# Kernel optimization log

Hardware: AMD Instinct MI355X
Metric: run time of the kernel (lower is better)

The kernel has to match this reference:

```python
import jax, jax.numpy as jnp
import numpy as np

N_QUBITS = 16
DIM = 1 << N_QUBITS
NUM_CLASSES = 23
BATCH = 64

# PauliZ sign table: wire 0 is the most-significant bit of the flattened index.
_idx = np.arange(DIM)
SIGNS = np.stack([1 - 2 * ((_idx >> (N_QUBITS - 1 - w)) & 1) for w in range(N_QUBITS)], axis=1).astype(np.float32)  # (DIM, 16)


def _rx_mat(theta):
    c = jnp.cos(theta / 2).astype(jnp.complex64)
    s = (-1j * jnp.sin(theta / 2)).astype(jnp.complex64)
    return jnp.stack([jnp.stack([c, s]), jnp.stack([s, c])])  # (2,2)


def _rot_mat(phi, theta, omega):
    ct = jnp.cos(theta / 2)
    st = jnp.sin(theta / 2)
    a = jnp.exp(-0.5j * (phi + omega)) * ct
    b = -jnp.exp(0.5j * (phi - omega)) * st
    c = jnp.exp(-0.5j * (phi - omega)) * st
    d = jnp.exp(0.5j * (phi + omega)) * ct
    return jnp.stack([jnp.stack([a, b]), jnp.stack([c, d])]).astype(jnp.complex64)


def _apply_1q(state, U, w):
    # state: (B, 2,...,2); shared 2x2 gate on wire w (axis w+1)
    st = jnp.tensordot(state, U, axes=[[w + 1], [1]])  # contracted axis moves to last
    return jnp.moveaxis(st, -1, w + 1)


def _apply_rx_batched(state, theta_b, w):
    # per-sample RX angles theta_b: (B,)
    half = theta_b / 2
    c = jnp.cos(half).astype(jnp.complex64)
    s = (-1j * jnp.sin(half)).astype(jnp.complex64)
    U = jnp.stack([jnp.stack([c, s], -1), jnp.stack([s, c], -1)], -2)  # (B,2,2)
    st = jnp.moveaxis(state, w + 1, -1)
    st = jnp.einsum('bji,b...i->b...j', U, st)
    return jnp.moveaxis(st, -1, w + 1)


def _apply_crx(state, theta, ctrl, tgt):
    s0 = jax.lax.index_in_dim(state, 0, axis=ctrl + 1, keepdims=False)
    s1 = jax.lax.index_in_dim(state, 1, axis=ctrl + 1, keepdims=False)
    tax = tgt + 1 if tgt < ctrl else tgt  # target axis after control axis removal
    U = _rx_mat(theta)
    s1 = jnp.moveaxis(jnp.tensordot(s1, U, axes=[[tax], [1]]), -1, tax)
    return jnp.stack([s0, s1], axis=ctrl + 1)


def _circuit(x, w0, x0, w1, x1):
    B = x.shape[0]
    state = jnp.zeros((B,) + (2,) * N_QUBITS, jnp.complex64)
    state = state.at[(slice(None),) + (0,) * N_QUBITS].set(1.0)
    for w, xc in ((w0, x0), (w1, x1)):
        for q in range(N_QUBITS):
            state = _apply_rx_batched(state, x[:, q], q)
        for q in range(N_QUBITS):
            state = _apply_1q(state, _rot_mat(w[q, 0], w[q, 1], w[q, 2]), q)
        for q in range(N_QUBITS):
            state = _apply_crx(state, xc[q], q, (q + 1) % N_QUBITS)
    probs = (state.real ** 2 + state.imag ** 2).reshape(B, DIM)
    return probs @ jnp.asarray(SIGNS)  # (B, 16) PauliZ expvals


def setup_inputs() -> dict:
    key = jax.random.key(0)
    ks = jax.random.split(key, 7)
    return {
        'x': jax.random.normal(ks[0], (BATCH, N_QUBITS), jnp.float32),
        'w0': jax.random.normal(ks[1], (N_QUBITS, 3), jnp.float32),
        'x0': jax.random.normal(ks[2], (N_QUBITS,), jnp.float32),
        'w1': jax.random.normal(ks[3], (N_QUBITS, 3), jnp.float32),
        'x1': jax.random.normal(ks[4], (N_QUBITS,), jnp.float32),
        'fc_w': jax.random.normal(ks[5], (NUM_CLASSES, N_QUBITS), jnp.float32) * 0.25,
        'fc_b': jax.random.normal(ks[6], (NUM_CLASSES,), jnp.float32) * 0.05,
    }


def reference(x, w0, x0, w1, x1, fc_w, fc_b):
    feats = _circuit(x, w0, x0, w1, x1)           # (B, 16)
    logits = feats @ fc_w.T + fc_b                # (B, 23)
    return jax.nn.log_softmax(logits, axis=1)
```

## Files before the change

kernel.cpp:

```cpp
#include <hip/hip_runtime.h>
#include <hip/hip_bf16.h>


#define DIM 65536
#define BATCH 64
#define PSTR 548


template<int RB>
__device__ __forceinline__ void g1q_reg(float* sr, float* si, const float* U) {
  float u00r=U[0],u00i=U[1],u01r=U[2],u01i=U[3],u10r=U[4],u10i=U[5],u11r=U[6],u11i=U[7];
#pragma unroll
  for (int k = 0; k < 8; ++k) {
    int lo = k & ((1<<RB)-1);
    int j0 = ((k >> RB) << (RB+1)) | lo;
    int j1 = j0 | (1<<RB);
    float a0r=sr[j0], a0i=si[j0], a1r=sr[j1], a1i=si[j1];
    sr[j0] = u00r*a0r - u00i*a0i + u01r*a1r - u01i*a1i;
    si[j0] = u00r*a0i + u00i*a0r + u01r*a1i + u01i*a1r;
    sr[j1] = u10r*a0r - u10i*a0i + u11r*a1r - u11i*a1i;
    si[j1] = u10r*a0i + u10i*a0r + u11r*a1i + u11i*a1r;
  }
}

template<int RB, int CB>
__device__ __forceinline__ void gsel_reg_cc(float* sr, float* si, const float* M0, const float* M1) {
  float a0=M0[0],a1=M0[1],a2=M0[2],a3=M0[3],a4=M0[4],a5=M0[5],a6=M0[6],a7=M0[7];
  float b0=M1[0],b1=M1[1],b2=M1[2],b3=M1[3],b4=M1[4],b5=M1[5],b6=M1[6],b7=M1[7];
#pragma unroll
  for (int k = 0; k < 8; ++k) {
    int lo = k & ((1<<RB)-1);
    int j0 = ((k >> RB) << (RB+1)) | lo;
    int j1 = j0 | (1<<RB);
    const bool c = ((j0 >> CB) & 1) != 0;
    float u00r=c?b0:a0, u00i=c?b1:a1, u01r=c?b2:a2, u01i=c?b3:a3;
    float u10r=c?b4:a4, u10i=c?b5:a5, u11r=c?b6:a6, u11i=c?b7:a7;
    float p0r=sr[j0], p0i=si[j0], p1r=sr[j1], p1i=si[j1];
    sr[j0] = u00r*p0r - u00i*p0i + u01r*p1r - u01i*p1i;
    si[j0] = u00r*p0i + u00i*p0r + u01r*p1i + u01i*p1r;
    sr[j1] = u10r*p0r - u10i*p0i + u11r*p1r - u11i*p1i;
    si[j1] = u10r*p0i + u10i*p0r + u11r*p1i + u11i*p1r;
  }
}

template<int RB>
__device__ __forceinline__ void gsel_reg_pred(float* sr, float* si, const float* M0,
                                              const float* M1, bool ctrl) {
  float u[8];
#pragma unroll
  for (int e = 0; e < 8; ++e) u[e] = ctrl ? M1[e] : M0[e];
  g1q_reg<RB>(sr, si, u);
}

template<int LB, int CB>
__device__ __forceinline__ void gsel_lane_creg(float* sr, float* si, const float* M0,
                                               const float* M1, int lane) {
  int side = (lane >> LB) & 1;
  float d0r = side ? M0[6] : M0[0], d0i = side ? M0[7] : M0[1];
  float o0r = side ? M0[4] : M0[2], o0i = side ? M0[5] : M0[3];
  float d1r = side ? M1[6] : M1[0], d1i = side ? M1[7] : M1[1];
  float o1r = side ? M1[4] : M1[2], o1i = side ? M1[5] : M1[3];
#pragma unroll
  for (int j = 0; j < 16; ++j) {
    const bool c = ((j >> CB) & 1) != 0;
    float dr = c ? d1r : d0r, di = c ? d1i : d0i;
    float og = c ? o1r : o0r, oi = c ? o1i : o0i;
    float pr = __shfl_xor(sr[j], 1<<LB, 64);
    float pi = __shfl_xor(si[j], 1<<LB, 64);
    float mr = sr[j], mi = si[j];
    sr[j] = dr*mr - di*mi + og*pr - oi*pi;
    si[j] = dr*mi + di*mr + og*pi + oi*pr;
  }
}

template<int CB, int LB>
__device__ __forceinline__ void crx_reg_lane(float* sr, float* si, float c, float s) {
#pragma unroll
  for (int k = 0; k < 8; ++k) {
    int lo2 = k & ((1<<CB)-1);
    int j = ((((k >> CB) << (CB+1)) | lo2)) | (1<<CB);
    float pr = __shfl_xor(sr[j], 1<<LB, 64);
    float pi = __shfl_xor(si[j], 1<<LB, 64);
    float mr = sr[j], mi = si[j];
    sr[j] = c*mr + s*pi;
    si[j] = c*mi - s*pr;
  }
}

__device__ __forceinline__ int swz(int o) { return o ^ ((o>>4)&15) ^ ((o>>8)&15); }

__device__ __forceinline__ unsigned bfp(float r, float i) {
  unsigned ur = __float_as_uint(r), ui = __float_as_uint(i);
  ur = (ur + 0x7fffu + ((ur >> 16) & 1u)) >> 16;
  ui = (ui + 0x7fffu + ((ui >> 16) & 1u)) & 0xffff0000u;
  return (ur & 0xffffu) | ui;
}
__device__ __forceinline__ float bfr(unsigned u) { return __uint_as_float(u << 16); }
__device__ __forceinline__ float bfi(unsigned u) { return __uint_as_float(u & 0xffff0000u); }

#define MP(Pb, l, q, s) ((Pb) + (((l)*16+(q))*2+(s))*8)


__global__ __launch_bounds__(512) void pA(float4* __restrict__ cst4, float* __restrict__ P,
                                          const float* __restrict__ x, const float* __restrict__ w0,
                                          const float* __restrict__ x0, const float* __restrict__ w1,
                                          const float* __restrict__ x1, float* __restrict__ feats,
                                          int* __restrict__ ctr) {
  __shared__ float2 lds2[8192];
  int b = blockIdx.x;
  int t = threadIdx.x, lane = t & 63, wv = t >> 6;
  float* Pb = P + (size_t)b * PSTR;

  {
    float (*su)[8] = reinterpret_cast<float(*)[8]>(lds2);
    if (t < 16) feats[b*16 + t] = 0.f;
    if (t == 16) ctr[b] = 0;
    if (t < 32) {
      int l = t >> 4, q = t & 15;
      const float* W = (l ? w1 : w0) + q*3;
      float xa = 0.5f * x[b*16 + q];
      float cr = cosf(xa), sx = sinf(xa);
      float phi = W[0], th = W[1], om = W[2];
      float ct = cosf(0.5f*th), stt = sinf(0.5f*th);
      float po = 0.5f*(phi+om), pm = 0.5f*(phi-om);
      float ar =  cosf(po)*ct,  ai = -sinf(po)*ct;
      float br = -cosf(pm)*stt, bi = -sinf(pm)*stt;
      float cr2 = cosf(pm)*stt, ci2 = -sinf(pm)*stt;
      float dr =  cosf(po)*ct,  di =  sinf(po)*ct;
      float U[8];
      U[0] = ar*cr + bi*sx;   U[1] = ai*cr - br*sx;
      U[2] = ai*sx + br*cr;   U[3] = -ar*sx + bi*cr;
      U[4] = cr2*cr + di*sx;  U[5] = ci2*cr - dr*sx;
      U[6] = ci2*sx + dr*cr;  U[7] = -cr2*sx + di*cr;
      float* M0 = MP(Pb, l, q, 0);
      float* M1 = M0 + 8;
#pragma unroll
      for (int e = 0; e < 8; ++e) { M0[e] = U[e]; su[t][e] = U[e]; }
      if (q == 0) {
        float ang = l ? 0.5f*x0[15] : 0.f;
        float cg = cosf(ang), sg = sinf(ang);
        M1[0] =  cg*U[0] + sg*U[3];  M1[1] = cg*U[1] - sg*U[2];
        M1[2] =  sg*U[1] + cg*U[2];  M1[3] = -sg*U[0] + cg*U[3];
        M1[4] =  cg*U[4] + sg*U[7];  M1[5] = cg*U[5] - sg*U[6];
        M1[6] =  sg*U[5] + cg*U[6];  M1[7] = -sg*U[4] + cg*U[7];
      } else {
        float ang = 0.5f*(l ? x1[q-1] : x0[q-1]);
        float cg = cosf(ang), sg = sinf(ang);
        M1[0] = cg*U[0] + sg*U[5];  M1[1] = cg*U[1] - sg*U[4];
        M1[2] = cg*U[2] + sg*U[7];  M1[3] = cg*U[3] - sg*U[6];
        M1[4] = cg*U[4] + sg*U[1];  M1[5] = cg*U[5] - sg*U[0];
        M1[6] = cg*U[6] + sg*U[3];  M1[7] = cg*U[7] - sg*U[2];
      }
      if (t == 0) { Pb[546] = cosf(0.5f*x1[15]); Pb[547] = sinf(0.5f*x1[15]); }
    }
    __syncthreads();
    if (t == 0) {
      float T0r[8], T0i[8], T1r[8], T1i[8];
#pragma unroll
      for (int k = 0; k < 8; ++k) {
        int b2 = (k>>2)&1, b1 = (k>>1)&1, b0k = k&1;
        float xr = su[13][b2*4], xi = su[13][b2*4+1];
        float yr = su[14][b1*4], yi = su[14][b1*4+1];
        float zr = su[15][b0k*4], zi = su[15][b0k*4+1];
        float pr = xr*yr - xi*yi, pi = xr*yi + xi*yr;
        T0r[k] = pr*zr - pi*zi; T0i[k] = pr*zi + pi*zr;
      }
      float a12 = 0.5f*x0[12], c12 = cosf(a12), s12 = sinf(a12);
#pragma unroll
      for (int k = 0; k < 8; ++k) { T1r[k] = c12*T0r[k] + s12*T0i[k^4]; T1i[k] = c12*T0i[k] - s12*T0r[k^4]; }
      float a13 = 0.5f*x0[13], c13 = cosf(a13), s13 = sinf(a13);
      float n0r[8], n0i[8], n1r[8], n1i[8];
#pragma unroll
      for (int k = 0; k < 8; ++k) {
        if (k & 4) {
          n0r[k] = c13*T0r[k] + s13*T0i[k^2]; n0i[k] = c13*T0i[k] - s13*T0r[k^2];
          n1r[k] = c13*T1r[k] + s13*T1i[k^2]; n1i[k] = c13*T1i[k] - s13*T1r[k^2];
        } else { n0r[k]=T0r[k]; n0i[k]=T0i[k]; n1r[k]=T1r[k]; n1i[k]=T1i[k]; }
      }
      float a14 = 0.5f*x0[14], c14 = cosf(a14), s14 = sinf(a14);
      float* T0 = Pb + 512;
      float* T1 = Pb + 528;
#pragma unroll
      for (int k = 0; k < 8; ++k) {
        float r0, i0, r1, i1;
        if (k & 2) {
          r0 = c14*n0r[k] + s14*n0i[k^1]; i0 = c14*n0i[k] - s14*n0r[k^1];
          r1 = c14*n1r[k] + s14*n1i[k^1]; i1 = c14*n1i[k] - s14*n1r[k^1];
        } else { r0=n0r[k]; i0=n0i[k]; r1=n1r[k]; i1=n1i[k]; }
        T0[2*k] = r0; T0[2*k+1] = i0; T1[2*k] = r1; T1[2*k+1] = i1;
      }
    }
  }

  float sr[16], si[16];
#pragma unroll
  for (int r = 0; r < 16; ++r) { sr[r] = 0.f; si[r] = 0.f; }
  if (t == 0) sr[0] = 1.f;

  g1q_reg<3>(sr, si, MP(Pb,0,0,0));
  gsel_reg_cc<2,3>(sr, si, MP(Pb,0,1,0), MP(Pb,0,1,1));
  gsel_reg_cc<1,2>(sr, si, MP(Pb,0,2,0), MP(Pb,0,2,1));
  gsel_reg_cc<0,1>(sr, si, MP(Pb,0,3,0), MP(Pb,0,3,1));
  __syncthreads();
#pragma unroll
  for (int r = 0; r < 16; ++r) {
    int o = wv | (lane << 3) | (r << 9);
    lds2[swz(o)] = make_float2(sr[r], si[r]);
  }
  __syncthreads();
#pragma unroll
  for (int r = 0; r < 16; ++r) {
    int o = wv | (((lane>>4)&3) << 3) | (r << 5) | ((lane&15) << 9);
    float2 v = lds2[swz(o)]; sr[r] = v.x; si[r] = v.y;
  }
  gsel_reg_pred<3>(sr, si, MP(Pb,0,4,0), MP(Pb,0,4,1), (lane&1)!=0);
  gsel_reg_cc<2,3>(sr, si, MP(Pb,0,5,0), MP(Pb,0,5,1));
  gsel_reg_cc<1,2>(sr, si, MP(Pb,0,6,0), MP(Pb,0,6,1));
  gsel_reg_cc<0,1>(sr, si, MP(Pb,0,7,0), MP(Pb,0,7,1));
  __syncthreads();
#pragma unroll
  for (int r = 0; r < 16; ++r) {
    int o = wv | (((lane>>4)&3) << 3) | (r << 5) | ((lane&15) << 9);
    lds2[swz(o)] = make_float2(sr[r], si[r]);
  }
  __syncthreads();
#pragma unroll
  for (int r = 0; r < 16; ++r) {
    int o = (lane&1) | (r << 1) | (((lane>>1)&31) << 5) | (wv << 10);
    float2 v = lds2[swz(o)]; sr[r] = v.x; si[r] = v.y;
  }
  gsel_reg_pred<3>(sr, si, MP(Pb,0,8,0), MP(Pb,0,8,1), (lane&2)!=0);
  gsel_reg_cc<2,3>(sr, si, MP(Pb,0,9,0), MP(Pb,0,9,1));
  gsel_reg_cc<1,2>(sr, si, MP(Pb,0,10,0), MP(Pb,0,10,1));
  gsel_reg_cc<0,1>(sr, si, MP(Pb,0,11,0), MP(Pb,0,11,1));
  gsel_lane_creg<0,0>(sr, si, MP(Pb,0,12,0), MP(Pb,0,12,1), lane);
  __syncthreads();
#pragma unroll
  for (int r = 0; r < 16; ++r) {
    int o = (lane&1) | (r << 1) | (((lane>>1)&31) << 5) | (wv << 10);
    lds2[swz(o)] = make_float2(sr[r], si[r]);
  }
  __syncthreads();
#pragma unroll
  for (int r = 0; r < 16; ++r) {
    int o = ((wv>>2)&1) | (lane << 1) | ((wv&3) << 7) | (r << 9);
    float2 v = lds2[swz(o)]; sr[r] = v.x; si[r] = v.y;
  }
  {
    int base4 = (lane << 3) | ((wv&3) << 9) | (((wv>>2)&1) << 11);
    float4* dst = cst4 + (size_t)b*4096 + base4;
#pragma unroll
    for (int g = 0; g < 8; ++g)
      dst[g] = make_float4(sr[2*g], si[2*g], sr[2*g+1], si[2*g+1]);
  }
}


__global__ __launch_bounds__(512) void pB(unsigned* __restrict__ st, const float4* __restrict__ cst4,
                                          const float* __restrict__ P) {
  __shared__ float2 lds2[8192];
  int blk = blockIdx.x;
  int b = blk >> 3, m = blk & 7;
  int t = threadIdx.x, lane = t & 63, wv = t >> 6;
  const float* Pb = P + (size_t)b*PSTR;

  float sr[16], si[16];
  {
    const float4* src = cst4 + (size_t)b*4096 + ((lane << 3) | ((wv&3) << 9) | (((m>>2)&1) << 11));
    const float* Ts = ((m>>2)&1) ? (Pb + 528) : (Pb + 512);
    int k = ((wv>>2)&1) | ((m&1) << 1) | (((m>>1)&1) << 2);
    float tr = Ts[2*k], ti = Ts[2*k+1];
#pragma unroll
    for (int g = 0; g < 8; ++g) {
      float4 v = src[g];
      sr[2*g]   = tr*v.x - ti*v.y;  si[2*g]   = tr*v.y + ti*v.x;
      sr[2*g+1] = tr*v.z - ti*v.w;  si[2*g+1] = tr*v.w + ti*v.z;
    }
  }
  gsel_reg_pred<3>(sr, si, MP(Pb,1,0,0), MP(Pb,1,0,1), ((wv>>2)&1)!=0);
  gsel_reg_cc<2,3>(sr, si, MP(Pb,1,1,0), MP(Pb,1,1,1));
  gsel_reg_cc<1,2>(sr, si, MP(Pb,1,2,0), MP(Pb,1,2,1));
  gsel_reg_cc<0,1>(sr, si, MP(Pb,1,3,0), MP(Pb,1,3,1));
#pragma unroll
  for (int r = 0; r < 16; ++r) {
    int o = (lane&63) | ((wv&3) << 6) | (r << 8) | (((wv>>2)&1) << 12);
    lds2[swz(o)] = make_float2(sr[r], si[r]);
  }
  __syncthreads();
#pragma unroll
  for (int r = 0; r < 16; ++r) {
    int o = (lane&15) | (r << 4) | (((lane>>4)&3) << 8) | ((wv&3) << 10) | (((wv>>2)&1) << 12);
    float2 v = lds2[swz(o)]; sr[r] = v.x; si[r] = v.y;
  }
  gsel_reg_pred<3>(sr, si, MP(Pb,1,4,0), MP(Pb,1,4,1), (lane&16)!=0);
  gsel_reg_cc<2,3>(sr, si, MP(Pb,1,5,0), MP(Pb,1,5,1));
  gsel_reg_cc<1,2>(sr, si, MP(Pb,1,6,0), MP(Pb,1,6,1));
  gsel_reg_cc<0,1>(sr, si, MP(Pb,1,7,0), MP(Pb,1,7,1));
  __syncthreads();
#pragma unroll
  for (int r = 0; r < 16; ++r) {
    int o = (lane&15) | (r << 4) | (((lane>>4)&3) << 8) | ((wv&3) << 10) | (((wv>>2)&1) << 12);
    lds2[swz(o)] = make_float2(sr[r], si[r]);
  }
  __syncthreads();
#pragma unroll
  for (int r = 0; r < 16; ++r) {
    int o = r | ((lane&63) << 4) | ((wv&3) << 10) | (((wv>>2)&1) << 12);
    float2 v = lds2[swz(o)]; sr[r] = v.x; si[r] = v.y;
  }
  gsel_reg_pred<3>(sr, si, MP(Pb,1,8,0), MP(Pb,1,8,1), (lane&1)!=0);
  gsel_reg_cc<2,3>(sr, si, MP(Pb,1,9,0), MP(Pb,1,9,1));
  gsel_reg_cc<1,2>(sr, si, MP(Pb,1,10,0), MP(Pb,1,10,1));
  gsel_reg_cc<0,1>(sr, si, MP(Pb,1,11,0), MP(Pb,1,11,1));
  {
    int sbase = ((lane&63) << 4) | ((wv&3) << 10) | (((wv>>2)&1) << 12) | (m << 13);
    uint4* dst = (uint4*)(st + (size_t)b*DIM + sbase);
#pragma unroll
    for (int g = 0; g < 4; ++g)
      dst[g] = make_uint4(bfp(sr[4*g],si[4*g]), bfp(sr[4*g+1],si[4*g+1]),
                          bfp(sr[4*g+2],si[4*g+2]), bfp(sr[4*g+3],si[4*g+3]));
  }
}


__global__ __launch_bounds__(512) void p3(const unsigned* __restrict__ st, const float* __restrict__ P,
                                          float* __restrict__ feats, int* __restrict__ ctr,
                                          const float* __restrict__ fcw, const float* __restrict__ fcb,
                                          float* __restrict__ out) {
  int blk = blockIdx.x;
  int b = blk >> 3, n = blk & 7;
  int t = threadIdx.x, lane = t & 63, wv = t >> 6;
  const float* Pb = P + (size_t)b*PSTR;
  int base = (lane&31) | (wv << 5) | (n << 8) | ((lane>>5) << 11);
  const unsigned* S = st + (size_t)b*DIM + base;
  float sr[16], si[16];
#pragma unroll
  for (int r = 0; r < 16; ++r) { unsigned u = S[r << 12]; sr[r] = bfr(u); si[r] = bfi(u); }

  gsel_reg_pred<3>(sr, si, MP(Pb,1,12,0), MP(Pb,1,12,1), (lane&1)!=0);
  gsel_reg_cc<2,3>(sr, si, MP(Pb,1,13,0), MP(Pb,1,13,1));
  gsel_reg_cc<1,2>(sr, si, MP(Pb,1,14,0), MP(Pb,1,14,1));
  gsel_reg_cc<0,1>(sr, si, MP(Pb,1,15,0), MP(Pb,1,15,1));
  crx_reg_lane<0,5>(sr, si, Pb[546], Pb[547]);

  float tot=0.f, sA=0.f, sB=0.f, sC=0.f, sD=0.f;
#pragma unroll
  for (int r = 0; r < 16; ++r) {
    float p = sr[r]*sr[r] + si[r]*si[r];
    tot += p;
    sA += (r & 1) ? -p : p;
    sB += (r & 2) ? -p : p;
    sC += (r & 4) ? -p : p;
    sD += (r & 8) ? -p : p;
  }
  float f[16];
  f[15] = sA; f[14] = sB; f[13] = sC; f[12] = sD;
  f[11] = (lane&1)  ? -tot : tot;
  f[10] = (lane&2)  ? -tot : tot;
  f[9]  = (lane&4)  ? -tot : tot;
  f[8]  = (lane&8)  ? -tot : tot;
  f[7]  = (lane&16) ? -tot : tot;
  f[0]  = (lane&32) ? -tot : tot;
  f[6]  = (wv&1)    ? -tot : tot;
  f[5]  = (wv&2)    ? -tot : tot;
  f[4]  = (wv&4)    ? -tot : tot;
  f[3]  = (n&1)     ? -tot : tot;
  f[2]  = (n&2)     ? -tot : tot;
  f[1]  = (n&4)     ? -tot : tot;
#pragma unroll
  for (int w = 0; w < 16; ++w) {
#pragma unroll
    for (int off = 32; off; off >>= 1) f[w] += __shfl_xor(f[w], off, 64);
  }
  __shared__ float red[8][17];
  if (lane == 0) {
#pragma unroll
    for (int w = 0; w < 16; ++w) red[wv][w] = f[w];
  }
  __syncthreads();
  if (t < 16) {
    float acc = 0.f;
#pragma unroll
    for (int i = 0; i < 8; ++i) acc += red[i][t];
    atomicAdd(&feats[b*16 + t], acc);
  }

  __shared__ int flagS;
  __syncthreads();
  if (t == 0) { __threadfence(); flagS = atomicAdd(&ctr[b], 1); }
  __syncthreads();
  if (flagS == 7) {
    __shared__ float fs[16];
    __shared__ float lg[23];
    if (t < 16) fs[t] = __hip_atomic_load(&feats[b*16 + t], __ATOMIC_RELAXED, __HIP_MEMORY_SCOPE_AGENT);
    __syncthreads();
    if (t < 23) {
      float acc = fcb[t];
#pragma unroll
      for (int w = 0; w < 16; ++w) acc += fs[w] * fcw[t*16 + w];
      lg[t] = acc;
    }
    __syncthreads();
    if (t < 23) {
      float mx = -1e30f;
#pragma unroll
      for (int j = 0; j < 23; ++j) mx = fmaxf(mx, lg[j]);
      float Ssum = 0.f;
#pragma unroll
      for (int j = 0; j < 23; ++j) Ssum += expf(lg[j] - mx);
      out[b*23 + t] = lg[t] - mx - logf(Ssum);
    }
  }
}

extern "C" void kernel_launch(void* const* d_in, const int* in_sizes, int n_in,
                              void* d_out, int out_size, void* d_ws, size_t ws_size,
                              hipStream_t stream) {
  const float* x   = (const float*)d_in[0];
  const float* w0  = (const float*)d_in[1];
  const float* x0  = (const float*)d_in[2];
  const float* w1  = (const float*)d_in[3];
  const float* x1  = (const float*)d_in[4];
  const float* fcw = (const float*)d_in[5];
  const float* fcb = (const float*)d_in[6];
  float* out = (float*)d_out;

  char* ws = (char*)d_ws;
  unsigned* st  = (unsigned*)ws;
  float4* cst4  = (float4*)(ws + (size_t)BATCH * DIM * 4);
  float*  P     = (float*)((char*)cst4 + (size_t)BATCH * 8192 * 8);
  float*  feats = P + (size_t)BATCH * PSTR;
  int*    ctr   = (int*)(feats + BATCH*16);

  pA<<<BATCH, 512, 0, stream>>>(cst4, P, x, w0, x0, w1, x1, feats, ctr);
  pB<<<512, 512, 0, stream>>>(st, cst4, P);
  p3<<<512, 512, 0, stream>>>(st, P, feats, ctr, fcw, fcb, out);
  (void)in_sizes; (void)n_in; (void)out_size; (void)ws_size;
}
```

Before: 130.5 us.

## Fold layer-0 wire-12 gate into tail product factors, halve pA state

The layer-0 qubit-12 controlled gate (the lane-shuffle step plus its LDS transpose) is removed from pA. Because that gate acts on a factorised tail, it is folded into the precomputed product-state factor table T2, which pB applies when it loads the intermediate state. pA now handles a 4096-amplitude state with 256 threads, half the LDS, one fewer exchange round and half the global intermediate write and read. The cost is a larger per-sample parameter table and extra masking on the LDS index; correctness depends on the factorisation holding exactly.

```diff
diff --git a/kernel.cpp b/kernel.cpp
--- a/kernel.cpp
+++ b/kernel.cpp
@@ -4,7 +4,7 @@
 
 #define DIM 65536
 #define BATCH 64
-#define PSTR 548
+#define PSTR 580
 
 
 template<int RB>
@@ -52,27 +52,6 @@
   g1q_reg<RB>(sr, si, u);
 }
 
-template<int LB, int CB>
-__device__ __forceinline__ void gsel_lane_creg(float* sr, float* si, const float* M0,
-                                               const float* M1, int lane) {
-  int side = (lane >> LB) & 1;
-  float d0r = side ? M0[6] : M0[0], d0i = side ? M0[7] : M0[1];
-  float o0r = side ? M0[4] : M0[2], o0i = side ? M0[5] : M0[3];
-  float d1r = side ? M1[6] : M1[0], d1i = side ? M1[7] : M1[1];
-  float o1r = side ? M1[4] : M1[2], o1i = side ? M1[5] : M1[3];
-#pragma unroll
-  for (int j = 0; j < 16; ++j) {
-    const bool c = ((j >> CB) & 1) != 0;
-    float dr = c ? d1r : d0r, di = c ? d1i : d0i;
-    float og = c ? o1r : o0r, oi = c ? o1i : o0i;
-    float pr = __shfl_xor(sr[j], 1<<LB, 64);
-    float pi = __shfl_xor(si[j], 1<<LB, 64);
-    float mr = sr[j], mi = si[j];
-    sr[j] = dr*mr - di*mi + og*pr - oi*pi;
-    si[j] = dr*mi + di*mr + og*pi + oi*pr;
-  }
-}
-
 template<int CB, int LB>
 __device__ __forceinline__ void crx_reg_lane(float* sr, float* si, float c, float s) {
 #pragma unroll
@@ -101,12 +80,12 @@
 #define MP(Pb, l, q, s) ((Pb) + (((l)*16+(q))*2+(s))*8)
 
 
-__global__ __launch_bounds__(512) void pA(float4* __restrict__ cst4, float* __restrict__ P,
+__global__ __launch_bounds__(256) void pA(float2* __restrict__ pre2, float* __restrict__ P,
                                           const float* __restrict__ x, const float* __restrict__ w0,
                                           const float* __restrict__ x0, const float* __restrict__ w1,
                                           const float* __restrict__ x1, float* __restrict__ feats,
                                           int* __restrict__ ctr) {
-  __shared__ float2 lds2[8192];
+  __shared__ float2 lds2[4096];
   int b = blockIdx.x;
   int t = threadIdx.x, lane = t & 63, wv = t >> 6;
   float* Pb = P + (size_t)b * PSTR;
@@ -151,7 +130,7 @@
         M1[4] = cg*U[4] + sg*U[1];  M1[5] = cg*U[5] - sg*U[0];
         M1[6] = cg*U[6] + sg*U[3];  M1[7] = cg*U[7] - sg*U[2];
       }
-      if (t == 0) { Pb[546] = cosf(0.5f*x1[15]); Pb[547] = sinf(0.5f*x1[15]); }
+      if (t == 0) { Pb[576] = cosf(0.5f*x1[15]); Pb[577] = sinf(0.5f*x1[15]); }
     }
     __syncthreads();
     if (t == 0) {
@@ -178,8 +157,7 @@
         } else { n0r[k]=T0r[k]; n0i[k]=T0i[k]; n1r[k]=T1r[k]; n1i[k]=T1i[k]; }
       }
       float a14 = 0.5f*x0[14], c14 = cosf(a14), s14 = sinf(a14);
-      float* T0 = Pb + 512;
-      float* T1 = Pb + 528;
+      float Fr[2][8], Fi[2][8];
 #pragma unroll
       for (int k = 0; k < 8; ++k) {
         float r0, i0, r1, i1;
@@ -187,8 +165,25 @@
           r0 = c14*n0r[k] + s14*n0i[k^1]; i0 = c14*n0i[k] - s14*n0r[k^1];
           r1 = c14*n1r[k] + s14*n1i[k^1]; i1 = c14*n1i[k] - s14*n1r[k^1];
         } else { r0=n0r[k]; i0=n0i[k]; r1=n1r[k]; i1=n1i[k]; }
-        T0[2*k] = r0; T0[2*k+1] = i0; T1[2*k] = r1; T1[2*k+1] = i1;
+        Fr[0][k] = r0; Fi[0][k] = i0; Fr[1][k] = r1; Fi[1][k] = i1;
       }
+      const float* A = MP(Pb,0,12,0);
+      const float* B = MP(Pb,0,12,1);
+      float wr[2][2], wi[2][2];
+      wr[0][0] = A[0]; wi[0][0] = A[1];  wr[1][0] = A[4]; wi[1][0] = A[5];
+      wr[0][1] = B[0]; wi[0][1] = B[1];  wr[1][1] = B[4]; wi[1][1] = B[5];
+      float* T2 = Pb + 512;
+#pragma unroll
+      for (int j0 = 0; j0 < 2; ++j0)
+#pragma unroll
+        for (int j1 = 0; j1 < 2; ++j1)
+#pragma unroll
+          for (int k = 0; k < 8; ++k) {
+            float tr = Fr[j0][k], ti = Fi[j0][k];
+            float fr = wr[j0][j1], fi = wi[j0][j1];
+            T2[((j0*2 + j1)*8 + k)*2 + 0] = tr*fr - ti*fi;
+            T2[((j0*2 + j1)*8 + k)*2 + 1] = tr*fi + ti*fr;
+          }
     }
   }
 
@@ -204,14 +199,14 @@
   __syncthreads();
 #pragma unroll
   for (int r = 0; r < 16; ++r) {
-    int o = wv | (lane << 3) | (r << 9);
-    lds2[swz(o)] = make_float2(sr[r], si[r]);
-  }
-  __syncthreads();
-#pragma unroll
-  for (int r = 0; r < 16; ++r) {
-    int o = wv | (((lane>>4)&3) << 3) | (r << 5) | ((lane&15) << 9);
-    float2 v = lds2[swz(o)]; sr[r] = v.x; si[r] = v.y;
+    int o = wv | (lane << 2) | (r << 8);
+    lds2[swz(o) & 4095] = make_float2(sr[r], si[r]);
+  }
+  __syncthreads();
+#pragma unroll
+  for (int r = 0; r < 16; ++r) {
+    int o = wv | (((lane>>4)&3) << 2) | (r << 4) | ((lane&15) << 8);
+    float2 v = lds2[swz(o) & 4095]; sr[r] = v.x; si[r] = v.y;
   }
   gsel_reg_pred<3>(sr, si, MP(Pb,0,4,0), MP(Pb,0,4,1), (lane&1)!=0);
   gsel_reg_cc<2,3>(sr, si, MP(Pb,0,5,0), MP(Pb,0,5,1));
@@ -220,43 +215,28 @@
   __syncthreads();
 #pragma unroll
   for (int r = 0; r < 16; ++r) {
-    int o = wv | (((lane>>4)&3) << 3) | (r << 5) | ((lane&15) << 9);
-    lds2[swz(o)] = make_float2(sr[r], si[r]);
-  }
-  __syncthreads();
-#pragma unroll
-  for (int r = 0; r < 16; ++r) {
-    int o = (lane&1) | (r << 1) | (((lane>>1)&31) << 5) | (wv << 10);
-    float2 v = lds2[swz(o)]; sr[r] = v.x; si[r] = v.y;
-  }
-  gsel_reg_pred<3>(sr, si, MP(Pb,0,8,0), MP(Pb,0,8,1), (lane&2)!=0);
+    int o = wv | (((lane>>4)&3) << 2) | (r << 4) | ((lane&15) << 8);
+    lds2[swz(o) & 4095] = make_float2(sr[r], si[r]);
+  }
+  __syncthreads();
+#pragma unroll
+  for (int r = 0; r < 16; ++r) {
+    int o = r | (lane << 4) | (wv << 10);
+    float2 v = lds2[swz(o) & 4095]; sr[r] = v.x; si[r] = v.y;
+  }
+  gsel_reg_pred<3>(sr, si, MP(Pb,0,8,0), MP(Pb,0,8,1), (lane&1)!=0);
   gsel_reg_cc<2,3>(sr, si, MP(Pb,0,9,0), MP(Pb,0,9,1));
   gsel_reg_cc<1,2>(sr, si, MP(Pb,0,10,0), MP(Pb,0,10,1));
   gsel_reg_cc<0,1>(sr, si, MP(Pb,0,11,0), MP(Pb,0,11,1));
-  gsel_lane_creg<0,0>(sr, si, MP(Pb,0,12,0), MP(Pb,0,12,1), lane);
-  __syncthreads();
-#pragma unroll
-  for (int r = 0; r < 16; ++r) {
-    int o = (lane&1) | (r << 1) | (((lane>>1)&31) << 5) | (wv << 10);
-    lds2[swz(o)] = make_float2(sr[r], si[r]);
-  }
-  __syncthreads();
-#pragma unroll
-  for (int r = 0; r < 16; ++r) {
-    int o = ((wv>>2)&1) | (lane << 1) | ((wv&3) << 7) | (r << 9);
-    float2 v = lds2[swz(o)]; sr[r] = v.x; si[r] = v.y;
-  }
-  {
-    int base4 = (lane << 3) | ((wv&3) << 9) | (((wv>>2)&1) << 11);
-    float4* dst = cst4 + (size_t)b*4096 + base4;
-#pragma unroll
-    for (int g = 0; g < 8; ++g)
-      dst[g] = make_float4(sr[2*g], si[2*g], sr[2*g+1], si[2*g+1]);
-  }
-}
-
-
-__global__ __launch_bounds__(512) void pB(unsigned* __restrict__ st, const float4* __restrict__ cst4,
+#pragma unroll
+  for (int r = 0; r < 16; ++r) {
+    int paddr = ((lane>>4)&3) | (wv << 2) | (r << 4) | ((lane&15) << 8);
+    pre2[(size_t)b*4096 + paddr] = make_float2(sr[r], si[r]);
+  }
+}
+
+
+__global__ __launch_bounds__(512) void pB(unsigned* __restrict__ st, const float2* __restrict__ pre2,
                                           const float* __restrict__ P) {
   __shared__ float2 lds2[8192];
   int blk = blockIdx.x;
@@ -266,15 +246,15 @@
 
   float sr[16], si[16];
   {
-    const float4* src = cst4 + (size_t)b*4096 + ((lane << 3) | ((wv&3) << 9) | (((m>>2)&1) << 11));
-    const float* Ts = ((m>>2)&1) ? (Pb + 528) : (Pb + 512);
-    int k = ((wv>>2)&1) | ((m&1) << 1) | (((m>>1)&1) << 2);
-    float tr = Ts[2*k], ti = Ts[2*k+1];
+    const float4* src = (const float4*)(pre2 + (size_t)b*4096) + ((lane << 3) | ((wv&3) << 9));
+    int k = ((wv>>2)&1) | ((m&3) << 1);
+    const float* tf = Pb + 512 + ((((m>>2)&1)*2 + (lane&1))*8 + k)*2;
+    float fr = tf[0], fi = tf[1];
 #pragma unroll
     for (int g = 0; g < 8; ++g) {
       float4 v = src[g];
-      sr[2*g]   = tr*v.x - ti*v.y;  si[2*g]   = tr*v.y + ti*v.x;
-      sr[2*g+1] = tr*v.z - ti*v.w;  si[2*g+1] = tr*v.w + ti*v.z;
+      sr[2*g]   = fr*v.x - fi*v.y;  si[2*g]   = fr*v.y + fi*v.x;
+      sr[2*g+1] = fr*v.z - fi*v.w;  si[2*g+1] = fr*v.w + fi*v.z;
     }
   }
   gsel_reg_pred<3>(sr, si, MP(Pb,1,0,0), MP(Pb,1,0,1), ((wv>>2)&1)!=0);
@@ -284,13 +264,13 @@
 #pragma unroll
   for (int r = 0; r < 16; ++r) {
     int o = (lane&63) | ((wv&3) << 6) | (r << 8) | (((wv>>2)&1) << 12);
-    lds2[swz(o)] = make_float2(sr[r], si[r]);
+    lds2[swz(o) & 8191] = make_float2(sr[r], si[r]);
   }
   __syncthreads();
 #pragma unroll
   for (int r = 0; r < 16; ++r) {
     int o = (lane&15) | (r << 4) | (((lane>>4)&3) << 8) | ((wv&3) << 10) | (((wv>>2)&1) << 12);
-    float2 v = lds2[swz(o)]; sr[r] = v.x; si[r] = v.y;
+    float2 v = lds2[swz(o) & 8191]; sr[r] = v.x; si[r] = v.y;
   }
   gsel_reg_pred<3>(sr, si, MP(Pb,1,4,0), MP(Pb,1,4,1), (lane&16)!=0);
   gsel_reg_cc<2,3>(sr, si, MP(Pb,1,5,0), MP(Pb,1,5,1));
@@ -300,13 +280,13 @@
 #pragma unroll
   for (int r = 0; r < 16; ++r) {
     int o = (lane&15) | (r << 4) | (((lane>>4)&3) << 8) | ((wv&3) << 10) | (((wv>>2)&1) << 12);
-    lds2[swz(o)] = make_float2(sr[r], si[r]);
+    lds2[swz(o) & 8191] = make_float2(sr[r], si[r]);
   }
   __syncthreads();
 #pragma unroll
   for (int r = 0; r < 16; ++r) {
     int o = r | ((lane&63) << 4) | ((wv&3) << 10) | (((wv>>2)&1) << 12);
-    float2 v = lds2[swz(o)]; sr[r] = v.x; si[r] = v.y;
+    float2 v = lds2[swz(o) & 8191]; sr[r] = v.x; si[r] = v.y;
   }
   gsel_reg_pred<3>(sr, si, MP(Pb,1,8,0), MP(Pb,1,8,1), (lane&1)!=0);
   gsel_reg_cc<2,3>(sr, si, MP(Pb,1,9,0), MP(Pb,1,9,1));
@@ -341,7 +321,7 @@
   gsel_reg_cc<2,3>(sr, si, MP(Pb,1,13,0), MP(Pb,1,13,1));
   gsel_reg_cc<1,2>(sr, si, MP(Pb,1,14,0), MP(Pb,1,14,1));
   gsel_reg_cc<0,1>(sr, si, MP(Pb,1,15,0), MP(Pb,1,15,1));
-  crx_reg_lane<0,5>(sr, si, Pb[546], Pb[547]);
+  crx_reg_lane<0,5>(sr, si, Pb[576], Pb[577]);
 
   float tot=0.f, sA=0.f, sB=0.f, sC=0.f, sD=0.f;
 #pragma unroll
@@ -427,13 +407,13 @@
 
   char* ws = (char*)d_ws;
   unsigned* st  = (unsigned*)ws;
-  float4* cst4  = (float4*)(ws + (size_t)BATCH * DIM * 4);
-  float*  P     = (float*)((char*)cst4 + (size_t)BATCH * 8192 * 8);
+  float2* pre2  = (float2*)(ws + (size_t)BATCH * DIM * 4);
+  float*  P     = (float*)((char*)pre2 + (size_t)BATCH * 4096 * 8);
   float*  feats = P + (size_t)BATCH * PSTR;
   int*    ctr   = (int*)(feats + BATCH*16);
 
-  pA<<<BATCH, 512, 0, stream>>>(cst4, P, x, w0, x0, w1, x1, feats, ctr);
-  pB<<<512, 512, 0, stream>>>(st, cst4, P);
+  pA<<<BATCH, 256, 0, stream>>>(pre2, P, x, w0, x0, w1, x1, feats, ctr);
+  pB<<<512, 512, 0, stream>>>(st, pre2, P);
   p3<<<512, 512, 0, stream>>>(st, P, feats, ctr, fcw, fcb, out);
   (void)in_sizes; (void)n_in; (void)out_size; (void)ws_size;
 }
```

After: 125.7 us. 1.04x faster.
